# Performance work log

Hardware: AMD Instinct MI355X
Metric: run time of the kernel (lower is better)

The kernel has to match this reference:

```python
import jax, jax.numpy as jnp
import numpy as np

T_BITS = 4
M_BITS = 4
T_MASK = (1 << T_BITS) - 1   # 15
M_MASK = (1 << M_BITS) - 1   # 15
ALPHA = 0.001


def _xor_reduce(x):
    # XOR tree reduction over axis 1 (static shapes, mirrors _xor_reduce_dim).
    n = x.shape[1]
    while n > 1:
        if n % 2 == 1:
            x = jnp.concatenate([x, jnp.zeros((x.shape[0], 1), x.dtype)], axis=1)
            n += 1
        x = x[:, : n // 2] ^ x[:, n // 2 : n]
        n //= 2
    return x[:, 0]


def _layer_step(active_mask, prev_ids, delta_t, mem_fict, mem_phys,
                tau, v_th, syn_w, mem_map, dmap):
    # active_mask: [B, n_in] bool; delta_t: [B] int32
    ws = active_mask.astype(jnp.float32) @ syn_w                     # [B, n_out]
    decay = jnp.exp(-tau[None, :] * delta_t[:, None].astype(jnp.float32))
    mem_fict = mem_fict * decay + ws
    masked = jnp.where(active_mask, prev_ids[None, :], jnp.int32(0))
    acc = _xor_reduce(masked)                                        # [B]
    mem_phys = ((mem_phys ^ delta_t[:, None]) ^ (acc[:, None] & M_MASK)) & M_MASK
    n_out = tau.shape[0]
    v_vals = mem_map[jnp.arange(n_out), mem_phys]                    # gather LUT [B, n_out]
    active_next = v_vals >= v_th[None, :]
    delta = ALPHA * (mem_phys.astype(jnp.float32) - v_vals)
    rows = jnp.broadcast_to(jnp.arange(n_out), mem_phys.shape)
    dmap = dmap.at[rows, mem_phys].add(delta)                        # scatter-add LUT deltas
    return active_next, mem_fict, mem_phys, dmap


def setup_inputs() -> dict:
    key = jax.random.key(0)
    ks = jax.random.split(key, 12)
    B, T, P, X, Y = 128, 128, 2, 34, 34
    n_in, n_hid, n_out = P * X * Y, 2048, 10
    m = 1 << M_BITS
    return {
        "frames": jax.random.randint(ks[0], (B, T, P, X, Y), 0, 2, dtype=jnp.int32),
        "input_neuron_id": jnp.arange(n_in, dtype=jnp.int32),
        "tau0": jax.random.uniform(ks[1], (n_hid,), jnp.float32),
        "v_th0": jax.random.uniform(ks[2], (n_hid,), jnp.float32),
        "neuron_id0": jax.random.randint(ks[3], (n_hid,), 0, m, dtype=jnp.int32),
        "mem_map0": jax.nn.sigmoid(jax.random.normal(ks[4], (n_hid, m), jnp.float32)),
        "syn_w0": jax.random.uniform(ks[5], (n_in, n_hid), jnp.float32),
        "tau1": jax.random.uniform(ks[6], (n_out,), jnp.float32),
        "v_th1": jax.random.uniform(ks[7], (n_out,), jnp.float32),
        "neuron_id1": jax.random.randint(ks[8], (n_out,), 0, m, dtype=jnp.int32),
        "mem_map1": jax.nn.sigmoid(jax.random.normal(ks[9], (n_out, m), jnp.float32)),
        "syn_w1": jax.random.uniform(ks[10], (n_hid, n_out), jnp.float32),
    }


def reference(frames, input_neuron_id, tau0, v_th0, neuron_id0, mem_map0, syn_w0,
              tau1, v_th1, neuron_id1, mem_map1, syn_w1):
    B, T = frames.shape[0], frames.shape[1]
    n_hid, n_out = tau0.shape[0], tau1.shape[0]
    m = mem_map0.shape[1]

    def body(carry, xs):
        t, frame_t = xs
        t_last, mf0, mp0, mf1, mp1, d0, d1 = carry
        active_in = (frame_t > 0).reshape(B, -1)
        has = jnp.any(active_in)  # torch skips the whole timestep if no spikes
        delta_t = (t - t_last) & T_MASK
        a1, nmf0, nmp0, nd0 = _layer_step(active_in, input_neuron_id, delta_t,
                                          mf0, mp0, tau0, v_th0, syn_w0, mem_map0, d0)
        a2, nmf1, nmp1, nd1 = _layer_step(a1, neuron_id0, delta_t,
                                          mf1, mp1, tau1, v_th1, syn_w1, mem_map1, d1)
        sel = lambda new, old: jnp.where(has, new, old)
        carry = (sel(jnp.full_like(t_last, t), t_last),
                 sel(nmf0, mf0), sel(nmp0, mp0),
                 sel(nmf1, mf1), sel(nmp1, mp1),
                 sel(nd0, d0), sel(nd1, d1))
        spikes = jnp.where(has, a2, False).astype(jnp.float32)
        return carry, spikes

    init = (jnp.zeros((B,), jnp.int32),
            jnp.zeros((B, n_hid), jnp.float32), jnp.zeros((B, n_hid), jnp.int32),
            jnp.zeros((B, n_out), jnp.float32), jnp.zeros((B, n_out), jnp.int32),
            jnp.zeros((n_hid, m), jnp.float32), jnp.zeros((n_out, m), jnp.float32))
    ts = jnp.arange(T, dtype=jnp.int32)
    carry, spikes_t = jax.lax.scan(body, init, (ts, jnp.swapaxes(frames, 0, 1)))
    out_spikes = jnp.swapaxes(spikes_t, 0, 1)  # [B, T, n_out] dense spike raster
    d0, d1 = carry[5], carry[6]
    return out_spikes, d0, d1
```

## Files before the change

kernel.cpp:

```cpp
#include <hip/hip_runtime.h>


#define ALPHA_F 0.001f

typedef int iv4 __attribute__((ext_vector_type(4)));

__global__ __launch_bounds__(256) void frames_reduce_kernel(
    const iv4* __restrict__ frames4, unsigned char* __restrict__ accanyT,
    int* __restrict__ tabs,
    const float* __restrict__ v_th0, const int* __restrict__ neuron_id0,
    const float* __restrict__ mem_map0,
    const float* __restrict__ v_th1, const float* __restrict__ mem_map1,
    int n4, int n_hid, int n_out, int nblocks, int B, int T) {
  int tid = threadIdx.x;
  int wv = tid >> 6, lane = tid & 63;

  if ((int)blockIdx.x < nblocks) {
    int bt = blockIdx.x * 4 + wv;
    const iv4* fp = frames4 + (size_t)bt * n4;
    int i0 = (lane << 2) & 15;
    int x = 0, anyv = 0;
#pragma unroll 5
    for (int idx = lane; idx < n4; idx += 64) {
      iv4 f = __builtin_nontemporal_load(&fp[idx]);
      if (f.x > 0) { x ^= i0;       anyv = 1; }
      if (f.y > 0) { x ^= (i0 + 1); anyv = 1; }
      if (f.z > 0) { x ^= (i0 + 2); anyv = 1; }
      if (f.w > 0) { x ^= (i0 + 3); anyv = 1; }
    }
#pragma unroll
    for (int off = 32; off > 0; off >>= 1) {
      x ^= __shfl_xor(x, off);
      anyv |= __shfl_xor(anyv, off);
    }
    if (lane == 0) {
      int b = bt / T, t = bt % T;
      accanyT[t * B + b] = (unsigned char)((x & 15) | (anyv << 4));
    }
    return;
  }

  int part[16];
#pragma unroll
  for (int v = 0; v < 16; v++) part[v] = 0;
  for (int j = tid; j < n_hid; j += 256) {
    float vth = v_th0[j];
    int nid = neuron_id0[j];
    const float4* mm = (const float4*)(mem_map0 + (size_t)j * 16);
    float4 m0 = mm[0], m1 = mm[1], m2 = mm[2], m3 = mm[3];
    if (m0.x >= vth) part[0]  ^= nid;
    if (m0.y >= vth) part[1]  ^= nid;
    if (m0.z >= vth) part[2]  ^= nid;
    if (m0.w >= vth) part[3]  ^= nid;
    if (m1.x >= vth) part[4]  ^= nid;
    if (m1.y >= vth) part[5]  ^= nid;
    if (m1.z >= vth) part[6]  ^= nid;
    if (m1.w >= vth) part[7]  ^= nid;
    if (m2.x >= vth) part[8]  ^= nid;
    if (m2.y >= vth) part[9]  ^= nid;
    if (m2.z >= vth) part[10] ^= nid;
    if (m2.w >= vth) part[11] ^= nid;
    if (m3.x >= vth) part[12] ^= nid;
    if (m3.y >= vth) part[13] ^= nid;
    if (m3.z >= vth) part[14] ^= nid;
    if (m3.w >= vth) part[15] ^= nid;
  }
  __shared__ int sred[4][16];
#pragma unroll
  for (int v = 0; v < 16; v++) {
    int xv = part[v];
#pragma unroll
    for (int off = 32; off > 0; off >>= 1) xv ^= __shfl_xor(xv, off);
    if (lane == 0) sred[wv][v] = xv;
  }
  __syncthreads();
  if (tid < 16) {
    tabs[tid] = (sred[0][tid] ^ sred[1][tid] ^ sred[2][tid] ^ sred[3][tid]) & 15;
    int msk = 0;
    for (int k = 0; k < n_out; k++)
      if (mem_map1[k * 16 + tid] >= v_th1[k]) msk |= (1 << k);
    tabs[16 + tid] = msk;
  }
}

__global__ __launch_bounds__(256) void scan_kernel(
    const unsigned char* __restrict__ accanyT, const int* __restrict__ tabs,
    int* __restrict__ smask, int* __restrict__ counts, int B, int T) {
  int tid = threadIdx.x;
  int wv = tid >> 6, lane = tid & 63;

  __shared__ unsigned char accL[128 * 132];
  __shared__ unsigned short smL[128 * 132];
  __shared__ int sTab[32];
  __shared__ unsigned long long sHp[2];
  __shared__ int sredc0[4][16], sredc1[4][16];

  const int* g4 = (const int*)accanyT;
  int nd = (B * T) >> 2;
  for (int i = tid; i < nd; i += 256) {
    int t = i >> 5, k = i & 31;
    *(int*)&accL[t * 132 + (k << 2)] = g4[i];
  }
  if (tid < 32) sTab[tid] = tabs[tid];
  __syncthreads();

  int h = 0;
  if (tid < T) {
    const unsigned int* row = (const unsigned int*)&accL[tid * 132];
    unsigned int hh = 0;
#pragma unroll
    for (int k = 0; k < 32; k++) hh |= row[k];
    h = (hh & 0x10101010u) ? 1 : 0;
  }
  unsigned long long bal = __ballot(h);
  if (lane == 0 && wv < 2) sHp[wv] = bal;

  unsigned long long A1p = 0, P0 = 0, P1 = 0, P2 = 0, P3 = 0;
#pragma unroll
  for (int v = 0; v < 16; v++)
    A1p |= (unsigned long long)(sTab[v] & 15) << (v * 4);
#pragma unroll
  for (int v = 0; v < 4; v++) {
    P0 |= (unsigned long long)(sTab[16 + v] & 0xFFFF) << (v * 16);
    P1 |= (unsigned long long)(sTab[20 + v] & 0xFFFF) << (v * 16);
    P2 |= (unsigned long long)(sTab[24 + v] & 0xFFFF) << (v * 16);
    P3 |= (unsigned long long)(sTab[28 + v] & 0xFFFF) << (v * 16);
  }
  __syncthreads();
  unsigned long long Hp0 = sHp[0], Hp1 = sHp[1];

  int myc0[16], myc1[16];
#pragma unroll
  for (int v = 0; v < 16; v++) { myc0[v] = 0; myc1[v] = 0; }

  if (tid < B) {
    int s0 = 0, s1 = 0, tlast = 0;
    unsigned long long c0lo = 0, c0hi = 0, c1lo = 0, c1hi = 0;
    for (int t = 0; t < T; t++) {
      int mask = 0;
      int hasbit = (int)((t < 64 ? (Hp0 >> t) : (Hp1 >> (t - 64))) & 1);
      if (hasbit) {
        int a = accL[t * 132 + tid] & 15;
        int dt = (t - tlast) & 15;
        s0 ^= dt ^ a;
        unsigned long long inc0 = 1ULL << ((s0 & 7) * 8);
        c0lo += (s0 < 8) ? inc0 : 0;
        c0hi += (s0 < 8) ? 0 : inc0;
        s1 ^= dt ^ (int)((A1p >> (s0 * 4)) & 15);
        unsigned long long inc1 = 1ULL << ((s1 & 7) * 8);
        c1lo += (s1 < 8) ? inc1 : 0;
        c1hi += (s1 < 8) ? 0 : inc1;
        tlast = t;
        unsigned long long q = (s1 & 8) ? ((s1 & 4) ? P3 : P2)
                                        : ((s1 & 4) ? P1 : P0);
        mask = (int)((q >> ((s1 & 3) * 16)) & 0xFFFF);
      }
      smL[t * 132 + tid] = (unsigned short)mask;
    }
#pragma unroll
    for (int v = 0; v < 8; v++) {
      myc0[v]     = (int)((c0lo >> (v * 8)) & 0xFF);
      myc0[v + 8] = (int)((c0hi >> (v * 8)) & 0xFF);
      myc1[v]     = (int)((c1lo >> (v * 8)) & 0xFF);
      myc1[v + 8] = (int)((c1hi >> (v * 8)) & 0xFF);
    }
  }
  __syncthreads();

  for (int i = tid; i < B * T; i += 256) {
    int b = i >> 7, t = i & 127;
    smask[i] = (int)smL[t * 132 + b];
  }

#pragma unroll
  for (int v = 0; v < 16; v++) {
    int a0 = myc0[v], a1 = myc1[v];
#pragma unroll
    for (int off = 32; off > 0; off >>= 1) {
      a0 += __shfl_xor(a0, off);
      a1 += __shfl_xor(a1, off);
    }
    if (lane == 0) { sredc0[wv][v] = a0; sredc1[wv][v] = a1; }
  }
  __syncthreads();
  if (tid < 16) {
    counts[tid]      = sredc0[0][tid] + sredc0[1][tid] + sredc0[2][tid] + sredc0[3][tid];
    counts[16 + tid] = sredc1[0][tid] + sredc1[1][tid] + sredc1[2][tid] + sredc1[3][tid];
  }
}

__global__ __launch_bounds__(256) void output_kernel(
    const int* __restrict__ smask, const int* __restrict__ counts,
    const float* __restrict__ mem_map0, const float* __restrict__ mem_map1,
    float* __restrict__ out, int spikes_n, int d0_n, int d1_n, int n_out) {
  int idx = blockIdx.x * 256 + threadIdx.x;
  if (idx < spikes_n) {
    int k = idx % n_out;
    int bt = idx / n_out;
    out[idx] = (float)((smask[bt] >> k) & 1);
  } else if (idx < spikes_n + d0_n) {
    int i2 = idx - spikes_n;
    int v = i2 & 15;
    out[idx] = ALPHA_F * ((float)v - mem_map0[i2]) * (float)counts[v];
  } else if (idx < spikes_n + d0_n + d1_n) {
    int i3 = idx - spikes_n - d0_n;
    int v = i3 & 15;
    out[idx] = ALPHA_F * ((float)v - mem_map1[i3]) * (float)counts[16 + v];
  }
}

extern "C" void kernel_launch(void* const* d_in, const int* in_sizes, int n_in,
                              void* d_out, int out_size, void* d_ws, size_t ws_size,
                              hipStream_t stream) {
  const int*   frames     = (const int*)d_in[0];
  const float* v_th0      = (const float*)d_in[3];
  const int*   neuron_id0 = (const int*)d_in[4];
  const float* mem_map0   = (const float*)d_in[5];
  const float* v_th1      = (const float*)d_in[8];
  const float* mem_map1   = (const float*)d_in[10];

  const int n_in_neurons = in_sizes[1];
  const int n_hid        = in_sizes[2];
  const int n_out        = in_sizes[7];
  const int B            = 128;
  const int BT           = in_sizes[0] / n_in_neurons;
  const int T            = BT / B;

  unsigned char* accanyT = (unsigned char*)d_ws;
  int* smask  = (int*)(accanyT + BT);
  int* counts = smask + BT;
  int* tabs   = counts + 32;

  int nblocks = BT / 4;
  frames_reduce_kernel<<<nblocks + 1, 256, 0, stream>>>(
      (const iv4*)frames, accanyT, tabs, v_th0, neuron_id0, mem_map0,
      v_th1, mem_map1, n_in_neurons / 4, n_hid, n_out, nblocks, B, T);
  scan_kernel<<<1, 256, 0, stream>>>(accanyT, tabs, smask, counts, B, T);
  int total = BT * n_out + n_hid * 16 + n_out * 16;
  output_kernel<<<(total + 255) / 256, 256, 0, stream>>>(
      smask, counts, mem_map0, mem_map1, (float*)d_out,
      BT * n_out, n_hid * 16, n_out * 16, n_out);
}
```

Measured before the change: 264.1 us.

## Fuse reduce, scan and output kernels into one cooperative grid-synced kernel

Merges the three kernels into one cooperative kernel with 1024 persistent blocks. Frame reduction is grid-strided, then one block runs the serial scan and a second grid barrier precedes the output write. This removes two kernel launches and the global transpose of the scan mask. In exchange it adds two grid-wide syncs, caps parallelism for the bandwidth-bound frames read at 1024 blocks, and the whole grid idles during the single-block scan.

```diff
diff --git a/kernel.cpp b/kernel.cpp
--- a/kernel.cpp
+++ b/kernel.cpp
@@ -1,218 +1,223 @@
 #include <hip/hip_runtime.h>
+#include <hip/hip_cooperative_groups.h>
+
+namespace cg = cooperative_groups;
 
 
 #define ALPHA_F 0.001f
-
 typedef int iv4 __attribute__((ext_vector_type(4)));
 
-__global__ __launch_bounds__(256) void frames_reduce_kernel(
-    const iv4* __restrict__ frames4, unsigned char* __restrict__ accanyT,
-    int* __restrict__ tabs,
+__global__ __launch_bounds__(256, 4) void snn_fused_kernel(
+    const iv4* __restrict__ frames4,
+    unsigned char* __restrict__ accanyT, int* __restrict__ tabs,
+    int* __restrict__ smaskT, int* __restrict__ counts,
     const float* __restrict__ v_th0, const int* __restrict__ neuron_id0,
     const float* __restrict__ mem_map0,
     const float* __restrict__ v_th1, const float* __restrict__ mem_map1,
-    int n4, int n_hid, int n_out, int nblocks, int B, int T) {
+    float* __restrict__ out,
+    int n4, int n_hid, int n_out, int B, int T) {
+  cg::grid_group grid = cg::this_grid();
   int tid = threadIdx.x;
   int wv = tid >> 6, lane = tid & 63;
-
-  if ((int)blockIdx.x < nblocks) {
-    int bt = blockIdx.x * 4 + wv;
-    const iv4* fp = frames4 + (size_t)bt * n4;
-    int i0 = (lane << 2) & 15;
-    int x = 0, anyv = 0;
-#pragma unroll 5
-    for (int idx = lane; idx < n4; idx += 64) {
-      iv4 f = __builtin_nontemporal_load(&fp[idx]);
-      if (f.x > 0) { x ^= i0;       anyv = 1; }
-      if (f.y > 0) { x ^= (i0 + 1); anyv = 1; }
-      if (f.z > 0) { x ^= (i0 + 2); anyv = 1; }
-      if (f.w > 0) { x ^= (i0 + 3); anyv = 1; }
-    }
-#pragma unroll
-    for (int off = 32; off > 0; off >>= 1) {
-      x ^= __shfl_xor(x, off);
-      anyv |= __shfl_xor(anyv, off);
-    }
-    if (lane == 0) {
-      int b = bt / T, t = bt % T;
-      accanyT[t * B + b] = (unsigned char)((x & 15) | (anyv << 4));
-    }
-    return;
-  }
-
-  int part[16];
-#pragma unroll
-  for (int v = 0; v < 16; v++) part[v] = 0;
-  for (int j = tid; j < n_hid; j += 256) {
-    float vth = v_th0[j];
-    int nid = neuron_id0[j];
-    const float4* mm = (const float4*)(mem_map0 + (size_t)j * 16);
-    float4 m0 = mm[0], m1 = mm[1], m2 = mm[2], m3 = mm[3];
-    if (m0.x >= vth) part[0]  ^= nid;
-    if (m0.y >= vth) part[1]  ^= nid;
-    if (m0.z >= vth) part[2]  ^= nid;
-    if (m0.w >= vth) part[3]  ^= nid;
-    if (m1.x >= vth) part[4]  ^= nid;
-    if (m1.y >= vth) part[5]  ^= nid;
-    if (m1.z >= vth) part[6]  ^= nid;
-    if (m1.w >= vth) part[7]  ^= nid;
-    if (m2.x >= vth) part[8]  ^= nid;
-    if (m2.y >= vth) part[9]  ^= nid;
-    if (m2.z >= vth) part[10] ^= nid;
-    if (m2.w >= vth) part[11] ^= nid;
-    if (m3.x >= vth) part[12] ^= nid;
-    if (m3.y >= vth) part[13] ^= nid;
-    if (m3.z >= vth) part[14] ^= nid;
-    if (m3.w >= vth) part[15] ^= nid;
-  }
-  __shared__ int sred[4][16];
-#pragma unroll
-  for (int v = 0; v < 16; v++) {
-    int xv = part[v];
-#pragma unroll
-    for (int off = 32; off > 0; off >>= 1) xv ^= __shfl_xor(xv, off);
-    if (lane == 0) sred[wv][v] = xv;
-  }
-  __syncthreads();
-  if (tid < 16) {
-    tabs[tid] = (sred[0][tid] ^ sred[1][tid] ^ sred[2][tid] ^ sred[3][tid]) & 15;
-    int msk = 0;
-    for (int k = 0; k < n_out; k++)
-      if (mem_map1[k * 16 + tid] >= v_th1[k]) msk |= (1 << k);
-    tabs[16 + tid] = msk;
-  }
-}
-
-__global__ __launch_bounds__(256) void scan_kernel(
-    const unsigned char* __restrict__ accanyT, const int* __restrict__ tabs,
-    int* __restrict__ smask, int* __restrict__ counts, int B, int T) {
-  int tid = threadIdx.x;
-  int wv = tid >> 6, lane = tid & 63;
-
-  __shared__ unsigned char accL[128 * 132];
-  __shared__ unsigned short smL[128 * 132];
+  int nBlocks = (int)gridDim.x;
+  int BT = B * T;
+
+  __shared__ union {
+    int sred[4][16];
+    unsigned char accL[128 * 132];
+  } u;
   __shared__ int sTab[32];
   __shared__ unsigned long long sHp[2];
   __shared__ int sredc0[4][16], sredc1[4][16];
 
-  const int* g4 = (const int*)accanyT;
-  int nd = (B * T) >> 2;
-  for (int i = tid; i < nd; i += 256) {
-    int t = i >> 5, k = i & 31;
-    *(int*)&accL[t * 132 + (k << 2)] = g4[i];
-  }
-  if (tid < 32) sTab[tid] = tabs[tid];
-  __syncthreads();
-
-  int h = 0;
-  if (tid < T) {
-    const unsigned int* row = (const unsigned int*)&accL[tid * 132];
-    unsigned int hh = 0;
-#pragma unroll
-    for (int k = 0; k < 32; k++) hh |= row[k];
-    h = (hh & 0x10101010u) ? 1 : 0;
-  }
-  unsigned long long bal = __ballot(h);
-  if (lane == 0 && wv < 2) sHp[wv] = bal;
-
-  unsigned long long A1p = 0, P0 = 0, P1 = 0, P2 = 0, P3 = 0;
-#pragma unroll
-  for (int v = 0; v < 16; v++)
-    A1p |= (unsigned long long)(sTab[v] & 15) << (v * 4);
-#pragma unroll
-  for (int v = 0; v < 4; v++) {
-    P0 |= (unsigned long long)(sTab[16 + v] & 0xFFFF) << (v * 16);
-    P1 |= (unsigned long long)(sTab[20 + v] & 0xFFFF) << (v * 16);
-    P2 |= (unsigned long long)(sTab[24 + v] & 0xFFFF) << (v * 16);
-    P3 |= (unsigned long long)(sTab[28 + v] & 0xFFFF) << (v * 16);
-  }
-  __syncthreads();
-  unsigned long long Hp0 = sHp[0], Hp1 = sHp[1];
-
-  int myc0[16], myc1[16];
-#pragma unroll
-  for (int v = 0; v < 16; v++) { myc0[v] = 0; myc1[v] = 0; }
-
-  if (tid < B) {
-    int s0 = 0, s1 = 0, tlast = 0;
-    unsigned long long c0lo = 0, c0hi = 0, c1lo = 0, c1hi = 0;
-    for (int t = 0; t < T; t++) {
-      int mask = 0;
-      int hasbit = (int)((t < 64 ? (Hp0 >> t) : (Hp1 >> (t - 64))) & 1);
-      if (hasbit) {
-        int a = accL[t * 132 + tid] & 15;
-        int dt = (t - tlast) & 15;
-        s0 ^= dt ^ a;
-        unsigned long long inc0 = 1ULL << ((s0 & 7) * 8);
-        c0lo += (s0 < 8) ? inc0 : 0;
-        c0hi += (s0 < 8) ? 0 : inc0;
-        s1 ^= dt ^ (int)((A1p >> (s0 * 4)) & 15);
-        unsigned long long inc1 = 1ULL << ((s1 & 7) * 8);
-        c1lo += (s1 < 8) ? inc1 : 0;
-        c1hi += (s1 < 8) ? 0 : inc1;
-        tlast = t;
-        unsigned long long q = (s1 & 8) ? ((s1 & 4) ? P3 : P2)
-                                        : ((s1 & 4) ? P1 : P0);
-        mask = (int)((q >> ((s1 & 3) * 16)) & 0xFFFF);
-      }
-      smL[t * 132 + tid] = (unsigned short)mask;
-    }
-#pragma unroll
-    for (int v = 0; v < 8; v++) {
-      myc0[v]     = (int)((c0lo >> (v * 8)) & 0xFF);
-      myc0[v + 8] = (int)((c0hi >> (v * 8)) & 0xFF);
-      myc1[v]     = (int)((c1lo >> (v * 8)) & 0xFF);
-      myc1[v + 8] = (int)((c1hi >> (v * 8)) & 0xFF);
-    }
-  }
-  __syncthreads();
-
-  for (int i = tid; i < B * T; i += 256) {
-    int b = i >> 7, t = i & 127;
-    smask[i] = (int)smL[t * 132 + b];
-  }
-
-#pragma unroll
-  for (int v = 0; v < 16; v++) {
-    int a0 = myc0[v], a1 = myc1[v];
-#pragma unroll
-    for (int off = 32; off > 0; off >>= 1) {
-      a0 += __shfl_xor(a0, off);
-      a1 += __shfl_xor(a1, off);
-    }
-    if (lane == 0) { sredc0[wv][v] = a0; sredc1[wv][v] = a1; }
-  }
-  __syncthreads();
-  if (tid < 16) {
-    counts[tid]      = sredc0[0][tid] + sredc0[1][tid] + sredc0[2][tid] + sredc0[3][tid];
-    counts[16 + tid] = sredc1[0][tid] + sredc1[1][tid] + sredc1[2][tid] + sredc1[3][tid];
-  }
-}
-
-__global__ __launch_bounds__(256) void output_kernel(
-    const int* __restrict__ smask, const int* __restrict__ counts,
-    const float* __restrict__ mem_map0, const float* __restrict__ mem_map1,
-    float* __restrict__ out, int spikes_n, int d0_n, int d1_n, int n_out) {
-  int idx = blockIdx.x * 256 + threadIdx.x;
-  if (idx < spikes_n) {
-    int k = idx % n_out;
-    int bt = idx / n_out;
-    out[idx] = (float)((smask[bt] >> k) & 1);
-  } else if (idx < spikes_n + d0_n) {
-    int i2 = idx - spikes_n;
-    int v = i2 & 15;
-    out[idx] = ALPHA_F * ((float)v - mem_map0[i2]) * (float)counts[v];
-  } else if (idx < spikes_n + d0_n + d1_n) {
-    int i3 = idx - spikes_n - d0_n;
-    int v = i3 & 15;
-    out[idx] = ALPHA_F * ((float)v - mem_map1[i3]) * (float)counts[16 + v];
+  {
+    int gw = blockIdx.x * 4 + wv;
+    int nW = nBlocks * 4;
+    int i0 = (lane << 2) & 15;
+    for (int bt = gw; bt < BT; bt += nW) {
+      const iv4* fp = frames4 + (size_t)bt * n4;
+      int x = 0, anyv = 0;
+#pragma unroll 5
+      for (int idx = lane; idx < n4; idx += 64) {
+        iv4 f = __builtin_nontemporal_load(&fp[idx]);
+        if (f.x > 0) { x ^= i0;       anyv = 1; }
+        if (f.y > 0) { x ^= (i0 + 1); anyv = 1; }
+        if (f.z > 0) { x ^= (i0 + 2); anyv = 1; }
+        if (f.w > 0) { x ^= (i0 + 3); anyv = 1; }
+      }
+#pragma unroll
+      for (int off = 32; off > 0; off >>= 1) {
+        x ^= __shfl_xor(x, off);
+        anyv |= __shfl_xor(anyv, off);
+      }
+      if (lane == 0) {
+        int b = bt / T, t = bt % T;
+        accanyT[t * B + b] = (unsigned char)((x & 15) | (anyv << 4));
+      }
+    }
+  }
+
+  if ((int)blockIdx.x == nBlocks - 1) {
+    int part[16];
+#pragma unroll
+    for (int v = 0; v < 16; v++) part[v] = 0;
+    for (int j = tid; j < n_hid; j += 256) {
+      float vth = v_th0[j];
+      int nid = neuron_id0[j];
+      const float4* mm = (const float4*)(mem_map0 + (size_t)j * 16);
+      float4 m0 = mm[0], m1 = mm[1], m2 = mm[2], m3 = mm[3];
+      if (m0.x >= vth) part[0]  ^= nid;
+      if (m0.y >= vth) part[1]  ^= nid;
+      if (m0.z >= vth) part[2]  ^= nid;
+      if (m0.w >= vth) part[3]  ^= nid;
+      if (m1.x >= vth) part[4]  ^= nid;
+      if (m1.y >= vth) part[5]  ^= nid;
+      if (m1.z >= vth) part[6]  ^= nid;
+      if (m1.w >= vth) part[7]  ^= nid;
+      if (m2.x >= vth) part[8]  ^= nid;
+      if (m2.y >= vth) part[9]  ^= nid;
+      if (m2.z >= vth) part[10] ^= nid;
+      if (m2.w >= vth) part[11] ^= nid;
+      if (m3.x >= vth) part[12] ^= nid;
+      if (m3.y >= vth) part[13] ^= nid;
+      if (m3.z >= vth) part[14] ^= nid;
+      if (m3.w >= vth) part[15] ^= nid;
+    }
+#pragma unroll
+    for (int v = 0; v < 16; v++) {
+      int xv = part[v];
+#pragma unroll
+      for (int off = 32; off > 0; off >>= 1) xv ^= __shfl_xor(xv, off);
+      if (lane == 0) u.sred[wv][v] = xv;
+    }
+    __syncthreads();
+    if (tid < 16) {
+      tabs[tid] = (u.sred[0][tid] ^ u.sred[1][tid] ^ u.sred[2][tid] ^ u.sred[3][tid]) & 15;
+      int msk = 0;
+      for (int k = 0; k < n_out; k++)
+        if (mem_map1[k * 16 + tid] >= v_th1[k]) msk |= (1 << k);
+      tabs[16 + tid] = msk;
+    }
+  }
+
+  grid.sync();
+
+  if (blockIdx.x == 0) {
+    const int* g4 = (const int*)accanyT;
+    int nd = BT >> 2;
+    for (int i = tid; i < nd; i += 256) {
+      int t = i >> 5, k = i & 31;
+      *(int*)&u.accL[t * 132 + (k << 2)] = g4[i];
+    }
+    if (tid < 32) sTab[tid] = tabs[tid];
+    __syncthreads();
+
+    int h = 0;
+    if (tid < T) {
+      const unsigned int* row = (const unsigned int*)&u.accL[tid * 132];
+      unsigned int hh = 0;
+#pragma unroll
+      for (int k = 0; k < 32; k++) hh |= row[k];
+      h = (hh & 0x10101010u) ? 1 : 0;
+    }
+    unsigned long long bal = __ballot(h);
+    if (lane == 0 && wv < 2) sHp[wv] = bal;
+
+    unsigned long long A1p = 0, P0 = 0, P1 = 0, P2 = 0, P3 = 0;
+#pragma unroll
+    for (int v = 0; v < 16; v++)
+      A1p |= (unsigned long long)(sTab[v] & 15) << (v * 4);
+#pragma unroll
+    for (int v = 0; v < 4; v++) {
+      P0 |= (unsigned long long)(sTab[16 + v] & 0xFFFF) << (v * 16);
+      P1 |= (unsigned long long)(sTab[20 + v] & 0xFFFF) << (v * 16);
+      P2 |= (unsigned long long)(sTab[24 + v] & 0xFFFF) << (v * 16);
+      P3 |= (unsigned long long)(sTab[28 + v] & 0xFFFF) << (v * 16);
+    }
+    __syncthreads();
+    unsigned long long Hp0 = sHp[0], Hp1 = sHp[1];
+
+    int myc0[16], myc1[16];
+#pragma unroll
+    for (int v = 0; v < 16; v++) { myc0[v] = 0; myc1[v] = 0; }
+
+    if (tid < B) {
+      int s0 = 0, s1 = 0, tlast = 0;
+      unsigned long long c0lo = 0, c0hi = 0, c1lo = 0, c1hi = 0;
+      for (int t = 0; t < T; t++) {
+        int mask = 0;
+        int hasbit = (int)((t < 64 ? (Hp0 >> t) : (Hp1 >> (t - 64))) & 1);
+        if (hasbit) {
+          int a = u.accL[t * 132 + tid] & 15;
+          int dt = (t - tlast) & 15;
+          s0 ^= dt ^ a;
+          unsigned long long inc0 = 1ULL << ((s0 & 7) * 8);
+          c0lo += (s0 < 8) ? inc0 : 0;
+          c0hi += (s0 < 8) ? 0 : inc0;
+          s1 ^= dt ^ (int)((A1p >> (s0 * 4)) & 15);
+          unsigned long long inc1 = 1ULL << ((s1 & 7) * 8);
+          c1lo += (s1 < 8) ? inc1 : 0;
+          c1hi += (s1 < 8) ? 0 : inc1;
+          tlast = t;
+          unsigned long long q = (s1 & 8) ? ((s1 & 4) ? P3 : P2)
+                                          : ((s1 & 4) ? P1 : P0);
+          mask = (int)((q >> ((s1 & 3) * 16)) & 0xFFFF);
+        }
+        smaskT[t * B + tid] = mask;
+      }
+#pragma unroll
+      for (int v = 0; v < 8; v++) {
+        myc0[v]     = (int)((c0lo >> (v * 8)) & 0xFF);
+        myc0[v + 8] = (int)((c0hi >> (v * 8)) & 0xFF);
+        myc1[v]     = (int)((c1lo >> (v * 8)) & 0xFF);
+        myc1[v + 8] = (int)((c1hi >> (v * 8)) & 0xFF);
+      }
+    }
+
+#pragma unroll
+    for (int v = 0; v < 16; v++) {
+      int a0 = myc0[v], a1 = myc1[v];
+#pragma unroll
+      for (int off = 32; off > 0; off >>= 1) {
+        a0 += __shfl_xor(a0, off);
+        a1 += __shfl_xor(a1, off);
+      }
+      if (lane == 0) { sredc0[wv][v] = a0; sredc1[wv][v] = a1; }
+    }
+    __syncthreads();
+    if (tid < 16) {
+      counts[tid]      = sredc0[0][tid] + sredc0[1][tid] + sredc0[2][tid] + sredc0[3][tid];
+      counts[16 + tid] = sredc1[0][tid] + sredc1[1][tid] + sredc1[2][tid] + sredc1[3][tid];
+    }
+  }
+
+  grid.sync();
+
+  int spikes_n = BT * n_out;
+  int d0_n = n_hid * 16, d1_n = n_out * 16;
+  int total = spikes_n + d0_n + d1_n;
+  for (int idx = blockIdx.x * 256 + tid; idx < total; idx += nBlocks * 256) {
+    if (idx < spikes_n) {
+      int k = idx % n_out;
+      int bt = idx / n_out;
+      int b = bt >> 7, t = bt & 127;
+      out[idx] = (float)((smaskT[t * B + b] >> k) & 1);
+    } else if (idx < spikes_n + d0_n) {
+      int i2 = idx - spikes_n;
+      int v = i2 & 15;
+      out[idx] = ALPHA_F * ((float)v - mem_map0[i2]) * (float)counts[v];
+    } else {
+      int i3 = idx - spikes_n - d0_n;
+      int v = i3 & 15;
+      out[idx] = ALPHA_F * ((float)v - mem_map1[i3]) * (float)counts[16 + v];
+    }
   }
 }
 
 extern "C" void kernel_launch(void* const* d_in, const int* in_sizes, int n_in,
                               void* d_out, int out_size, void* d_ws, size_t ws_size,
                               hipStream_t stream) {
-  const int*   frames     = (const int*)d_in[0];
+  const iv4*   frames4    = (const iv4*)d_in[0];
   const float* v_th0      = (const float*)d_in[3];
   const int*   neuron_id0 = (const int*)d_in[4];
   const float* mem_map0   = (const float*)d_in[5];
@@ -220,24 +225,25 @@
   const float* mem_map1   = (const float*)d_in[10];
 
   const int n_in_neurons = in_sizes[1];
-  const int n_hid        = in_sizes[2];
-  const int n_out        = in_sizes[7];
-  const int B            = 128;
-  const int BT           = in_sizes[0] / n_in_neurons;
-  const int T            = BT / B;
+  int n_hid        = in_sizes[2];
+  int n_out        = in_sizes[7];
+  int B            = 128;
+  const int BT     = in_sizes[0] / n_in_neurons;
+  int T            = BT / B;
+  int n4           = n_in_neurons / 4;
 
   unsigned char* accanyT = (unsigned char*)d_ws;
-  int* smask  = (int*)(accanyT + BT);
-  int* counts = smask + BT;
+  int* smaskT = (int*)(accanyT + BT);
+  int* counts = smaskT + BT;
   int* tabs   = counts + 32;
-
-  int nblocks = BT / 4;
-  frames_reduce_kernel<<<nblocks + 1, 256, 0, stream>>>(
-      (const iv4*)frames, accanyT, tabs, v_th0, neuron_id0, mem_map0,
-      v_th1, mem_map1, n_in_neurons / 4, n_hid, n_out, nblocks, B, T);
-  scan_kernel<<<1, 256, 0, stream>>>(accanyT, tabs, smask, counts, B, T);
-  int total = BT * n_out + n_hid * 16 + n_out * 16;
-  output_kernel<<<(total + 255) / 256, 256, 0, stream>>>(
-      smask, counts, mem_map0, mem_map1, (float*)d_out,
-      BT * n_out, n_hid * 16, n_out * 16, n_out);
+  float* out  = (float*)d_out;
+
+  void* args[] = {
+    (void*)&frames4, (void*)&accanyT, (void*)&tabs, (void*)&smaskT, (void*)&counts,
+    (void*)&v_th0, (void*)&neuron_id0, (void*)&mem_map0,
+    (void*)&v_th1, (void*)&mem_map1, (void*)&out,
+    (void*)&n4, (void*)&n_hid, (void*)&n_out, (void*)&B, (void*)&T,
+  };
+  hipLaunchCooperativeKernel((const void*)snn_fused_kernel,
+                             dim3(1024), dim3(256), args, 0, stream);
 }
```

New measurement: 491.9 us. 86.2% more time.

## Fuse frame reduction and serial scan via last-block-done atomic counter

Applied to the files above, without the earlier changes.

Merges the frame reduction kernel and the single-block scan kernel into one launch. The last block to finish, detected with an atomic counter and thread fences, runs the sequential scan. The scan now writes spike masks straight to global memory in [T,B] order instead of staging them in shared memory and transposing, and the output kernel indexes that layout. This removes one kernel launch and its gap, plus the shared-memory transpose. In exchange it adds a memset launch for the counter and leaves the serial scan on a single block's tail.

```diff
diff --git a/kernel.cpp b/kernel.cpp
--- a/kernel.cpp
+++ b/kernel.cpp
@@ -5,15 +5,25 @@
 
 typedef int iv4 __attribute__((ext_vector_type(4)));
 
-__global__ __launch_bounds__(256) void frames_reduce_kernel(
+__global__ __launch_bounds__(256) void snn_stream_scan(
     const iv4* __restrict__ frames4, unsigned char* __restrict__ accanyT,
-    int* __restrict__ tabs,
+    int* __restrict__ tabs, int* __restrict__ smaskT, int* __restrict__ counts,
+    int* __restrict__ done,
     const float* __restrict__ v_th0, const int* __restrict__ neuron_id0,
     const float* __restrict__ mem_map0,
     const float* __restrict__ v_th1, const float* __restrict__ mem_map1,
     int n4, int n_hid, int n_out, int nblocks, int B, int T) {
   int tid = threadIdx.x;
   int wv = tid >> 6, lane = tid & 63;
+
+  __shared__ union {
+    int sred[4][16];
+    unsigned char accL[128 * 132];
+  } u;
+  __shared__ int sTab[32];
+  __shared__ unsigned long long sHp[2];
+  __shared__ int sredc0[4][16], sredc1[4][16];
+  __shared__ int sOld;
 
   if ((int)blockIdx.x < nblocks) {
     int bt = blockIdx.x * 4 + wv;
@@ -37,76 +47,70 @@
       int b = bt / T, t = bt % T;
       accanyT[t * B + b] = (unsigned char)((x & 15) | (anyv << 4));
     }
-    return;
-  }
-
-  int part[16];
-#pragma unroll
-  for (int v = 0; v < 16; v++) part[v] = 0;
-  for (int j = tid; j < n_hid; j += 256) {
-    float vth = v_th0[j];
-    int nid = neuron_id0[j];
-    const float4* mm = (const float4*)(mem_map0 + (size_t)j * 16);
-    float4 m0 = mm[0], m1 = mm[1], m2 = mm[2], m3 = mm[3];
-    if (m0.x >= vth) part[0]  ^= nid;
-    if (m0.y >= vth) part[1]  ^= nid;
-    if (m0.z >= vth) part[2]  ^= nid;
-    if (m0.w >= vth) part[3]  ^= nid;
-    if (m1.x >= vth) part[4]  ^= nid;
-    if (m1.y >= vth) part[5]  ^= nid;
-    if (m1.z >= vth) part[6]  ^= nid;
-    if (m1.w >= vth) part[7]  ^= nid;
-    if (m2.x >= vth) part[8]  ^= nid;
-    if (m2.y >= vth) part[9]  ^= nid;
-    if (m2.z >= vth) part[10] ^= nid;
-    if (m2.w >= vth) part[11] ^= nid;
-    if (m3.x >= vth) part[12] ^= nid;
-    if (m3.y >= vth) part[13] ^= nid;
-    if (m3.z >= vth) part[14] ^= nid;
-    if (m3.w >= vth) part[15] ^= nid;
-  }
-  __shared__ int sred[4][16];
-#pragma unroll
-  for (int v = 0; v < 16; v++) {
-    int xv = part[v];
-#pragma unroll
-    for (int off = 32; off > 0; off >>= 1) xv ^= __shfl_xor(xv, off);
-    if (lane == 0) sred[wv][v] = xv;
-  }
-  __syncthreads();
-  if (tid < 16) {
-    tabs[tid] = (sred[0][tid] ^ sred[1][tid] ^ sred[2][tid] ^ sred[3][tid]) & 15;
-    int msk = 0;
-    for (int k = 0; k < n_out; k++)
-      if (mem_map1[k * 16 + tid] >= v_th1[k]) msk |= (1 << k);
-    tabs[16 + tid] = msk;
-  }
-}
-
-__global__ __launch_bounds__(256) void scan_kernel(
-    const unsigned char* __restrict__ accanyT, const int* __restrict__ tabs,
-    int* __restrict__ smask, int* __restrict__ counts, int B, int T) {
-  int tid = threadIdx.x;
-  int wv = tid >> 6, lane = tid & 63;
-
-  __shared__ unsigned char accL[128 * 132];
-  __shared__ unsigned short smL[128 * 132];
-  __shared__ int sTab[32];
-  __shared__ unsigned long long sHp[2];
-  __shared__ int sredc0[4][16], sredc1[4][16];
-
-  const int* g4 = (const int*)accanyT;
-  int nd = (B * T) >> 2;
-  for (int i = tid; i < nd; i += 256) {
-    int t = i >> 5, k = i & 31;
-    *(int*)&accL[t * 132 + (k << 2)] = g4[i];
-  }
-  if (tid < 32) sTab[tid] = tabs[tid];
+  } else {
+    int part[16];
+#pragma unroll
+    for (int v = 0; v < 16; v++) part[v] = 0;
+    for (int j = tid; j < n_hid; j += 256) {
+      float vth = v_th0[j];
+      int nid = neuron_id0[j];
+      const float4* mm = (const float4*)(mem_map0 + (size_t)j * 16);
+      float4 m0 = mm[0], m1 = mm[1], m2 = mm[2], m3 = mm[3];
+      if (m0.x >= vth) part[0]  ^= nid;
+      if (m0.y >= vth) part[1]  ^= nid;
+      if (m0.z >= vth) part[2]  ^= nid;
+      if (m0.w >= vth) part[3]  ^= nid;
+      if (m1.x >= vth) part[4]  ^= nid;
+      if (m1.y >= vth) part[5]  ^= nid;
+      if (m1.z >= vth) part[6]  ^= nid;
+      if (m1.w >= vth) part[7]  ^= nid;
+      if (m2.x >= vth) part[8]  ^= nid;
+      if (m2.y >= vth) part[9]  ^= nid;
+      if (m2.z >= vth) part[10] ^= nid;
+      if (m2.w >= vth) part[11] ^= nid;
+      if (m3.x >= vth) part[12] ^= nid;
+      if (m3.y >= vth) part[13] ^= nid;
+      if (m3.z >= vth) part[14] ^= nid;
+      if (m3.w >= vth) part[15] ^= nid;
+    }
+#pragma unroll
+    for (int v = 0; v < 16; v++) {
+      int xv = part[v];
+#pragma unroll
+      for (int off = 32; off > 0; off >>= 1) xv ^= __shfl_xor(xv, off);
+      if (lane == 0) u.sred[wv][v] = xv;
+    }
+    __syncthreads();
+    if (tid < 16) {
+      tabs[tid] = (u.sred[0][tid] ^ u.sred[1][tid] ^ u.sred[2][tid] ^ u.sred[3][tid]) & 15;
+      int msk = 0;
+      for (int k = 0; k < n_out; k++)
+        if (mem_map1[k * 16 + tid] >= v_th1[k]) msk |= (1 << k);
+      tabs[16 + tid] = msk;
+    }
+  }
+
+  __syncthreads();
+  __threadfence();
+  if (tid == 0) sOld = atomicAdd(done, 1);
+  __syncthreads();
+  if (sOld != nblocks) return;
+  __threadfence();
+
+  {
+    const int* g4 = (const int*)accanyT;
+    int nd = (B * T) >> 2;
+    for (int i = tid; i < nd; i += 256) {
+      int t = i >> 5, k = i & 31;
+      *(int*)&u.accL[t * 132 + (k << 2)] = g4[i];
+    }
+    if (tid < 32) sTab[tid] = tabs[tid];
+  }
   __syncthreads();
 
   int h = 0;
   if (tid < T) {
-    const unsigned int* row = (const unsigned int*)&accL[tid * 132];
+    const unsigned int* row = (const unsigned int*)&u.accL[tid * 132];
     unsigned int hh = 0;
 #pragma unroll
     for (int k = 0; k < 32; k++) hh |= row[k];
@@ -140,7 +144,7 @@
       int mask = 0;
       int hasbit = (int)((t < 64 ? (Hp0 >> t) : (Hp1 >> (t - 64))) & 1);
       if (hasbit) {
-        int a = accL[t * 132 + tid] & 15;
+        int a = u.accL[t * 132 + tid] & 15;
         int dt = (t - tlast) & 15;
         s0 ^= dt ^ a;
         unsigned long long inc0 = 1ULL << ((s0 & 7) * 8);
@@ -155,7 +159,7 @@
                                         : ((s1 & 4) ? P1 : P0);
         mask = (int)((q >> ((s1 & 3) * 16)) & 0xFFFF);
       }
-      smL[t * 132 + tid] = (unsigned short)mask;
+      smaskT[t * B + tid] = mask;
     }
 #pragma unroll
     for (int v = 0; v < 8; v++) {
@@ -165,12 +169,6 @@
       myc1[v + 8] = (int)((c1hi >> (v * 8)) & 0xFF);
     }
   }
-  __syncthreads();
-
-  for (int i = tid; i < B * T; i += 256) {
-    int b = i >> 7, t = i & 127;
-    smask[i] = (int)smL[t * 132 + b];
-  }
 
 #pragma unroll
   for (int v = 0; v < 16; v++) {
@@ -190,14 +188,15 @@
 }
 
 __global__ __launch_bounds__(256) void output_kernel(
-    const int* __restrict__ smask, const int* __restrict__ counts,
+    const int* __restrict__ smaskT, const int* __restrict__ counts,
     const float* __restrict__ mem_map0, const float* __restrict__ mem_map1,
-    float* __restrict__ out, int spikes_n, int d0_n, int d1_n, int n_out) {
+    float* __restrict__ out, int spikes_n, int d0_n, int d1_n, int n_out, int B, int T) {
   int idx = blockIdx.x * 256 + threadIdx.x;
   if (idx < spikes_n) {
     int k = idx % n_out;
     int bt = idx / n_out;
-    out[idx] = (float)((smask[bt] >> k) & 1);
+    int b = bt / T, t = bt % T;
+    out[idx] = (float)((smaskT[t * B + b] >> k) & 1);
   } else if (idx < spikes_n + d0_n) {
     int i2 = idx - spikes_n;
     int v = i2 & 15;
@@ -227,17 +226,20 @@
   const int T            = BT / B;
 
   unsigned char* accanyT = (unsigned char*)d_ws;
-  int* smask  = (int*)(accanyT + BT);
-  int* counts = smask + BT;
+  int* smaskT = (int*)(accanyT + BT);
+  int* counts = smaskT + BT;
   int* tabs   = counts + 32;
+  int* done   = tabs + 32;
+
+  hipMemsetAsync(done, 0, sizeof(int), stream);
 
   int nblocks = BT / 4;
-  frames_reduce_kernel<<<nblocks + 1, 256, 0, stream>>>(
-      (const iv4*)frames, accanyT, tabs, v_th0, neuron_id0, mem_map0,
-      v_th1, mem_map1, n_in_neurons / 4, n_hid, n_out, nblocks, B, T);
-  scan_kernel<<<1, 256, 0, stream>>>(accanyT, tabs, smask, counts, B, T);
+  snn_stream_scan<<<nblocks + 1, 256, 0, stream>>>(
+      (const iv4*)frames, accanyT, tabs, smaskT, counts, done,
+      v_th0, neuron_id0, mem_map0, v_th1, mem_map1,
+      n_in_neurons / 4, n_hid, n_out, nblocks, B, T);
   int total = BT * n_out + n_hid * 16 + n_out * 16;
   output_kernel<<<(total + 255) / 256, 256, 0, stream>>>(
-      smask, counts, mem_map0, mem_map1, (float*)d_out,
-      BT * n_out, n_hid * 16, n_out * 16, n_out);
+      smaskT, counts, mem_map0, mem_map1, (float*)d_out,
+      BT * n_out, n_hid * 16, n_out * 16, n_out, B, T);
 }
```

Result: slower. 786.0 us (+197.6%).

## Fuse scan and output kernels with redundant per-block scan

Applied to the files above, without the earlier changes.

Merges the single-block scan kernel and the output kernel into one launch of 192 blocks. Each block redundantly recomputes the full sequential scan in shared memory and then writes its grid-stride slice of the spike raster and LUT deltas straight from shared memory. This removes one kernel launch and the global round-trip of smask and counts, at the cost of repeating the serial scan in every block.

```diff
diff --git a/kernel.cpp b/kernel.cpp
--- a/kernel.cpp
+++ b/kernel.cpp
@@ -83,9 +83,10 @@
   }
 }
 
-__global__ __launch_bounds__(256) void scan_kernel(
+__global__ __launch_bounds__(256) void scan_output_kernel(
     const unsigned char* __restrict__ accanyT, const int* __restrict__ tabs,
-    int* __restrict__ smask, int* __restrict__ counts, int B, int T) {
+    const float* __restrict__ mem_map0, const float* __restrict__ mem_map1,
+    float* __restrict__ out, int B, int T, int n_hid, int n_out) {
   int tid = threadIdx.x;
   int wv = tid >> 6, lane = tid & 63;
 
@@ -94,6 +95,7 @@
   __shared__ int sTab[32];
   __shared__ unsigned long long sHp[2];
   __shared__ int sredc0[4][16], sredc1[4][16];
+  __shared__ int sCnt[32];
 
   const int* g4 = (const int*)accanyT;
   int nd = (B * T) >> 2;
@@ -165,12 +167,6 @@
       myc1[v + 8] = (int)((c1hi >> (v * 8)) & 0xFF);
     }
   }
-  __syncthreads();
-
-  for (int i = tid; i < B * T; i += 256) {
-    int b = i >> 7, t = i & 127;
-    smask[i] = (int)smL[t * 132 + b];
-  }
 
 #pragma unroll
   for (int v = 0; v < 16; v++) {
@@ -184,28 +180,29 @@
   }
   __syncthreads();
   if (tid < 16) {
-    counts[tid]      = sredc0[0][tid] + sredc0[1][tid] + sredc0[2][tid] + sredc0[3][tid];
-    counts[16 + tid] = sredc1[0][tid] + sredc1[1][tid] + sredc1[2][tid] + sredc1[3][tid];
-  }
-}
-
-__global__ __launch_bounds__(256) void output_kernel(
-    const int* __restrict__ smask, const int* __restrict__ counts,
-    const float* __restrict__ mem_map0, const float* __restrict__ mem_map1,
-    float* __restrict__ out, int spikes_n, int d0_n, int d1_n, int n_out) {
-  int idx = blockIdx.x * 256 + threadIdx.x;
-  if (idx < spikes_n) {
-    int k = idx % n_out;
-    int bt = idx / n_out;
-    out[idx] = (float)((smask[bt] >> k) & 1);
-  } else if (idx < spikes_n + d0_n) {
-    int i2 = idx - spikes_n;
-    int v = i2 & 15;
-    out[idx] = ALPHA_F * ((float)v - mem_map0[i2]) * (float)counts[v];
-  } else if (idx < spikes_n + d0_n + d1_n) {
-    int i3 = idx - spikes_n - d0_n;
-    int v = i3 & 15;
-    out[idx] = ALPHA_F * ((float)v - mem_map1[i3]) * (float)counts[16 + v];
+    sCnt[tid]      = sredc0[0][tid] + sredc0[1][tid] + sredc0[2][tid] + sredc0[3][tid];
+    sCnt[16 + tid] = sredc1[0][tid] + sredc1[1][tid] + sredc1[2][tid] + sredc1[3][tid];
+  }
+  __syncthreads();
+
+  int spikes_n = B * T * n_out;
+  int d0_n = n_hid * 16, d1_n = n_out * 16;
+  int total = spikes_n + d0_n + d1_n;
+  for (int idx = blockIdx.x * 256 + tid; idx < total; idx += (int)gridDim.x * 256) {
+    if (idx < spikes_n) {
+      int k = idx % n_out;
+      int bt = idx / n_out;
+      int b = bt >> 7, t = bt & 127;
+      out[idx] = (float)((smL[t * 132 + b] >> k) & 1);
+    } else if (idx < spikes_n + d0_n) {
+      int i2 = idx - spikes_n;
+      int v = i2 & 15;
+      out[idx] = ALPHA_F * ((float)v - mem_map0[i2]) * (float)sCnt[v];
+    } else {
+      int i3 = idx - spikes_n - d0_n;
+      int v = i3 & 15;
+      out[idx] = ALPHA_F * ((float)v - mem_map1[i3]) * (float)sCnt[16 + v];
+    }
   }
 }
 
@@ -227,17 +224,12 @@
   const int T            = BT / B;
 
   unsigned char* accanyT = (unsigned char*)d_ws;
-  int* smask  = (int*)(accanyT + BT);
-  int* counts = smask + BT;
-  int* tabs   = counts + 32;
+  int* tabs   = (int*)(accanyT + BT);
 
   int nblocks = BT / 4;
   frames_reduce_kernel<<<nblocks + 1, 256, 0, stream>>>(
       (const iv4*)frames, accanyT, tabs, v_th0, neuron_id0, mem_map0,
       v_th1, mem_map1, n_in_neurons / 4, n_hid, n_out, nblocks, B, T);
-  scan_kernel<<<1, 256, 0, stream>>>(accanyT, tabs, smask, counts, B, T);
-  int total = BT * n_out + n_hid * 16 + n_out * 16;
-  output_kernel<<<(total + 255) / 256, 256, 0, stream>>>(
-      smask, counts, mem_map0, mem_map1, (float*)d_out,
-      BT * n_out, n_hid * 16, n_out * 16, n_out);
+  scan_output_kernel<<<192, 256, 0, stream>>>(
+      accanyT, tabs, mem_map0, mem_map1, (float*)d_out, B, T, n_hid, n_out);
 }
```

Result: faster. 258.6 us (-2.1%).
